# Performance work log

Measured on AMD Instinct MI355X. Metric: run time of the kernel, lower is better.

## Reference

```python
import jax, jax.numpy as jnp
import numpy as np

EPS = 1e-5  # torch BatchNorm1d default eps
O, T, D, H1, H2 = 8, 4, 256, 64, 32


def setup_inputs() -> dict:
    key = jax.random.key(0)
    ks = jax.random.split(key, 8)
    B = 65536
    feature = jax.random.normal(ks[0], (B, D), dtype=jnp.float32)
    treatment = jax.random.randint(ks[1], (B,), 0, T, dtype=jnp.int64)
    s1 = 1.0 / np.sqrt(D)
    s2 = 1.0 / np.sqrt(H1)
    s3 = 1.0 / np.sqrt(H2)
    params = {
        # per (outcome, treatment) expert MLP weights
        'W1': jax.random.uniform(ks[2], (O, T, D, H1), jnp.float32, -s1, s1),
        'b1': jnp.zeros((O, T, H1), jnp.float32),
        'g1': jnp.ones((O, T, H1), jnp.float32),   # BN1 gamma
        'be1': jnp.zeros((O, T, H1), jnp.float32),  # BN1 beta
        'm1': jnp.zeros((O, T, H1), jnp.float32),   # BN1 running mean
        'v1': jnp.ones((O, T, H1), jnp.float32),    # BN1 running var
        'W2': jax.random.uniform(ks[3], (O, T, H1, H2), jnp.float32, -s2, s2),
        'b2': jnp.zeros((O, T, H2), jnp.float32),
        'g2': jnp.ones((O, T, H2), jnp.float32),
        'be2': jnp.zeros((O, T, H2), jnp.float32),
        'm2': jnp.zeros((O, T, H2), jnp.float32),
        'v2': jnp.ones((O, T, H2), jnp.float32),
        'W3': jax.random.uniform(ks[4], (O, T, H2), jnp.float32, -s3, s3),  # final Linear(32,1), squeezed
        'b3': jnp.zeros((O, T), jnp.float32),
    }
    return {'feature': feature, 'treatment': treatment, **params}


def _tlearner_fwd(x, t, W1, b1, g1, be1, m1, v1, W2, b2, g2, be2, m2, v2, W3, b3):
    # Dense evaluation of every (outcome, treatment) expert, then per-row
    # selection by treatment id. Equivalent (in eval mode: BN uses running
    # stats, dropout off) to the masked dispatch of the original module.
    h = jnp.einsum('bd,otdh->both', x, W1) + b1          # [B,O,T,H1]
    h = jax.nn.relu(h)
    h = (h - m1) * jax.lax.rsqrt(v1 + EPS) * g1 + be1    # BN1 (eval)
    h = jnp.einsum('both,othk->botk', h, W2) + b2        # [B,O,T,H2]
    h = jax.nn.relu(h)
    h = (h - m2) * jax.lax.rsqrt(v2 + EPS) * g2 + be2    # BN2 (eval)
    out = jnp.einsum('botk,otk->bot', h, W3) + b3        # [B,O,T]
    idx = t.astype(jnp.int32)[:, None, None]             # [B,1,1]
    return jnp.take_along_axis(out, jnp.broadcast_to(idx, (out.shape[0], O, 1)), axis=2)[..., 0]  # [B,O]


def reference(feature, treatment, W1, b1, g1, be1, m1, v1, W2, b2, g2, be2, m2, v2, W3, b3):
    return _tlearner_fwd(feature, treatment, W1, b1, g1, be1, m1, v1,
                         W2, b2, g2, be2, m2, v2, W3, b3)
```

## Files before the change

kernel.cpp:

```cpp
#include <hip/hip_runtime.h>
#include <cstdint>

typedef short bf16x8 __attribute__((ext_vector_type(8)));
typedef float f32x4 __attribute__((ext_vector_type(4)));

#define NO 8
#define NT 4
#define ND 256
#define NH1 64
#define NH2 32
#define BM 64
#define BNEPS 1e-5f

__device__ __forceinline__ unsigned bfpack2(float a, float b) {
    unsigned ua = __float_as_uint(a), ub = __float_as_uint(b);
    ua = (ua + 0x7FFFu + ((ua >> 16) & 1u)) >> 16;
    ub = (ub + 0x7FFFu + ((ub >> 16) & 1u)) >> 16;
    return ua | (ub << 16);
}


__global__ void k_init(int* __restrict__ ws, int* __restrict__ perm, int n) {
    const int gi = blockIdx.x * blockDim.x + threadIdx.x;
    if (gi < 16) ws[gi] = 0;
    if (gi < n) perm[gi] = -1;
}

__global__ void k_hist(const int* __restrict__ trt, int* __restrict__ cnt, int B) {
    __shared__ int loc[NT];
    const int tid = threadIdx.x;
    if (tid < NT) loc[tid] = 0;
    __syncthreads();
    const int i = blockIdx.x * blockDim.x + tid;
    if (i < B) atomicAdd(&loc[trt[i] & 3], 1);
    __syncthreads();
    if (tid < NT) atomicAdd(&cnt[tid], loc[tid]);
}

__global__ void k_prefix(int* __restrict__ ws) {
    int b = 0;
#pragma unroll
    for (int t = 0; t < NT; ++t) {
        ws[4 + t] = b; ws[12 + t] = b;
        b += (ws[t] + BM - 1) & ~(BM - 1);
    }
    ws[8] = b;
}

__global__ void k_scatter(const int* __restrict__ trt, int* __restrict__ ws,
                          int* __restrict__ perm, int B) {
    __shared__ int loc[NT], gb[NT];
    const int tid = threadIdx.x;
    if (tid < NT) loc[tid] = 0;
    __syncthreads();
    const int i = blockIdx.x * blockDim.x + tid;
    int tt = 0, pos = 0;
    if (i < B) { tt = trt[i] & 3; pos = atomicAdd(&loc[tt], 1); }
    __syncthreads();
    if (tid < NT) gb[tid] = atomicAdd(&ws[12 + tid], loc[tid]);
    __syncthreads();
    if (i < B) perm[gb[tt] + pos] = i;
}

__global__ __launch_bounds__(256) void k_prep(const float* __restrict__ W1,
                                              const float* __restrict__ W2,
                                              unsigned* __restrict__ W1T4,
                                              unsigned* __restrict__ W2T4) {
    const int bid = blockIdx.x, tid = threadIdx.x;
    if (bid < 256) {
        const int gi = bid * 256 + tid;
        const int lane = gi & 63, nt = (gi >> 6) & 31, c = (gi >> 11) & 7, t = gi >> 14;
        const int n16 = lane & 15, kg = lane >> 4;
        const int n = nt * 16 + n16, o = n >> 6, h = n & 63;
        const int k0 = c * 32 + kg * 8;
        const float* src = W1 + ((size_t)(o * NT + t) * ND + k0) * NH1 + h;
        float v[8];
#pragma unroll
        for (int j = 0; j < 8; ++j) v[j] = src[(size_t)j * NH1];
        uint4 q;
        q.x = bfpack2(v[0], v[1]); q.y = bfpack2(v[2], v[3]);
        q.z = bfpack2(v[4], v[5]); q.w = bfpack2(v[6], v[7]);
        ((uint4*)W1T4)[gi] = q;
    } else {
        const int gi = (bid - 256) * 256 + tid;
        const int m16 = gi & 15, kg = (gi >> 4) & 3, ks = (gi >> 6) & 1,
                  kt = (gi >> 7) & 1, o = (gi >> 8) & 7, t = gi >> 11;
        const int k2 = kt * 16 + m16, hb = ks * 32 + kg * 8;
        const float* src = W2 + ((size_t)(o * NT + t) * NH1 + hb) * NH2 + k2;
        float v[8];
#pragma unroll
        for (int j = 0; j < 8; ++j) v[j] = src[(size_t)j * NH2];
        uint4 q;
        q.x = bfpack2(v[0], v[1]); q.y = bfpack2(v[2], v[3]);
        q.z = bfpack2(v[4], v[5]); q.w = bfpack2(v[6], v[7]);
        ((uint4*)W2T4)[gi] = q;
    }
}

__global__ __launch_bounds__(256, 2) void k_main(
    const float* __restrict__ X, const int* __restrict__ ws, const int* __restrict__ perm,
    const unsigned short* __restrict__ W1T, const unsigned short* __restrict__ W2T,
    const float* __restrict__ pb1, const float* __restrict__ pg1, const float* __restrict__ pbe1,
    const float* __restrict__ pm1, const float* __restrict__ pv1,
    const float* __restrict__ pb2, const float* __restrict__ pg2, const float* __restrict__ pbe2,
    const float* __restrict__ pm2, const float* __restrict__ pv2,
    const float* __restrict__ W3, const float* __restrict__ pb3, float* __restrict__ out)
{
    const int m0 = blockIdx.x * BM;
    if (m0 >= ws[8]) return;
    const int t = (m0 >= ws[5]) + (m0 >= ws[6]) + (m0 >= ws[7]);
    const int tid = threadIdx.x;
    const int w = tid >> 6;
    const int l = tid & 63;

    __shared__ __align__(16) char LDS[75776];

    const int rid_reg = perm[m0 + l];
    const int xrow = tid >> 2;
    const int rr = __shfl(rid_reg, xrow);
    const int xdo = (tid & 3) * 8;

    f32x4 acc[8][4];
#pragma unroll
    for (int nt = 0; nt < 8; ++nt)
#pragma unroll
        for (int rt = 0; rt < 4; ++rt) acc[nt][rt] = (f32x4){0.f, 0.f, 0.f, 0.f};

    const char* W1Tt = (const char*)W1T + (size_t)t * 262144;
    const int ln4 = (l >> 4) * 4;

    {
#pragma unroll
        for (int u = 0; u < 8; ++u) {
            const int sl = (u * 4 + w) * 1024 + l * 16;
            __builtin_amdgcn_global_load_lds(
                (const __attribute__((address_space(1))) void*)(W1Tt + sl),
                (__attribute__((address_space(3))) void*)(LDS + sl), 16, 0, 0);
        }
        float4 xa = {0,0,0,0}, xb = {0,0,0,0};
        if (rr >= 0) {
            const float* xp = X + (size_t)rr * ND + xdo;
            xa = *(const float4*)xp; xb = *(const float4*)(xp + 4);
        }
        uint4 q;
        q.x = bfpack2(xa.x, xa.y); q.y = bfpack2(xa.z, xa.w);
        q.z = bfpack2(xb.x, xb.y); q.w = bfpack2(xb.z, xb.w);
        *(uint4*)(LDS + 65536 + xrow * 80 + (tid & 3) * 16) = q;
    }
    __syncthreads();

    int cur = 0;
    for (int c = 0; c < 8; ++c) {
        const int nxt = cur ^ 1;
        float4 xa = {0,0,0,0}, xb = {0,0,0,0};
        if (c < 7) {
            const char* src = W1Tt + (c + 1) * 32768;
#pragma unroll
            for (int u = 0; u < 8; ++u) {
                const int sl = (u * 4 + w) * 1024 + l * 16;
                __builtin_amdgcn_global_load_lds(
                    (const __attribute__((address_space(1))) void*)(src + sl),
                    (__attribute__((address_space(3))) void*)(LDS + nxt * 32768 + sl), 16, 0, 0);
            }
            if (rr >= 0) {
                const float* xp = X + (size_t)rr * ND + (c + 1) * 32 + xdo;
                xa = *(const float4*)xp; xb = *(const float4*)(xp + 4);
            }
        }
        bf16x8 aA[8];
#pragma unroll
        for (int nt = 0; nt < 8; ++nt)
            aA[nt] = *(const bf16x8*)(LDS + cur * 32768 + (w * 8 + nt) * 1024 + l * 16);
#pragma unroll
        for (int rt = 0; rt < 4; ++rt) {
            const bf16x8 bX = *(const bf16x8*)(LDS + 65536 + cur * 5120 +
                                               (rt * 16 + (l & 15)) * 80 + (l >> 4) * 16);
#pragma unroll
            for (int nt = 0; nt < 8; ++nt)
                acc[nt][rt] = __builtin_amdgcn_mfma_f32_16x16x32_bf16(aA[nt], bX, acc[nt][rt], 0, 0, 0);
        }
        if (c < 7) {
            uint4 q;
            q.x = bfpack2(xa.x, xa.y); q.y = bfpack2(xa.z, xa.w);
            q.z = bfpack2(xb.x, xb.y); q.w = bfpack2(xb.z, xb.w);
            *(uint4*)(LDS + 65536 + nxt * 5120 + xrow * 80 + (tid & 3) * 16) = q;
        }
        __syncthreads();
        cur = nxt;
    }

#pragma unroll
    for (int nt = 0; nt < 8; ++nt) {
        const int n0 = (w * 8 + nt) * 16 + ln4;
        const int o = n0 >> 6, h0 = n0 & 63;
        const int pidx = (o * NT + t) * NH1 + h0;
        const float4 b1v = *(const float4*)(pb1 + pidx);
        const float4 g1v = *(const float4*)(pg1 + pidx);
        const float4 be1v = *(const float4*)(pbe1 + pidx);
        const float4 m1v = *(const float4*)(pm1 + pidx);
        const float4 v1v = *(const float4*)(pv1 + pidx);
        float bb[4], sc[4], sh[4];
        bb[0] = b1v.x; sc[0] = g1v.x * rsqrtf(v1v.x + BNEPS); sh[0] = be1v.x - m1v.x * sc[0];
        bb[1] = b1v.y; sc[1] = g1v.y * rsqrtf(v1v.y + BNEPS); sh[1] = be1v.y - m1v.y * sc[1];
        bb[2] = b1v.z; sc[2] = g1v.z * rsqrtf(v1v.z + BNEPS); sh[2] = be1v.z - m1v.z * sc[2];
        bb[3] = b1v.w; sc[3] = g1v.w * rsqrtf(v1v.w + BNEPS); sh[3] = be1v.w - m1v.w * sc[3];
#pragma unroll
        for (int rt = 0; rt < 4; ++rt) {
            const int r = rt * 16 + (l & 15);
            const f32x4 a = acc[nt][rt];
            const float z0 = fmaf(fmaxf(a[0] + bb[0], 0.f), sc[0], sh[0]);
            const float z1 = fmaf(fmaxf(a[1] + bb[1], 0.f), sc[1], sh[1]);
            const float z2 = fmaf(fmaxf(a[2] + bb[2], 0.f), sc[2], sh[2]);
            const float z3 = fmaf(fmaxf(a[3] + bb[3], 0.f), sc[3], sh[3]);
            uint2 pk;
            pk.x = bfpack2(z0, z1); pk.y = bfpack2(z2, z3);
            *(uint2*)(LDS + r * 1024 + (((unsigned)(n0 * 2)) ^ (unsigned)((r & 7) << 4))) = pk;
        }
    }

    bf16x8 aW[2][2][2];
#pragma unroll
    for (int oo = 0; oo < 2; ++oo) {
        const int o = w * 2 + oo;
#pragma unroll
        for (int kt = 0; kt < 2; ++kt)
#pragma unroll
            for (int ks = 0; ks < 2; ++ks)
                aW[oo][kt][ks] = *(const bf16x8*)((const char*)W2T +
                    ((((size_t)t * NO + o) * 2 + kt) * 2 + ks) * 1024 + l * 16);
    }
    f32x4 acc2[2][2][4];
#pragma unroll
    for (int oo = 0; oo < 2; ++oo)
#pragma unroll
        for (int kt = 0; kt < 2; ++kt)
#pragma unroll
            for (int rt2 = 0; rt2 < 4; ++rt2) acc2[oo][kt][rt2] = (f32x4){0.f, 0.f, 0.f, 0.f};

#pragma unroll
    for (int rt2 = 0; rt2 < 4; ++rt2) {
        const int r = rt2 * 16 + (l & 15);
        const unsigned swz = (unsigned)((r & 7) << 4);
#pragma unroll
        for (int ks = 0; ks < 2; ++ks) {
            const int nb = ks * 32 + (l >> 4) * 8;
#pragma unroll
            for (int oo = 0; oo < 2; ++oo) {
                const int n8 = (w * 2 + oo) * 64 + nb;
                const bf16x8 bH = *(const bf16x8*)(LDS + r * 1024 + (((unsigned)(n8 * 2)) ^ swz));
#pragma unroll
                for (int kt = 0; kt < 2; ++kt)
                    acc2[oo][kt][rt2] = __builtin_amdgcn_mfma_f32_16x16x32_bf16(aW[oo][kt][ks], bH, acc2[oo][kt][rt2], 0, 0, 0);
            }
        }
    }

    float p[2][4];
#pragma unroll
    for (int oo = 0; oo < 2; ++oo)
#pragma unroll
        for (int rt2 = 0; rt2 < 4; ++rt2) p[oo][rt2] = 0.f;

#pragma unroll
    for (int oo = 0; oo < 2; ++oo) {
        const int o = w * 2 + oo;
#pragma unroll
        for (int kt = 0; kt < 2; ++kt) {
            const int k2 = kt * 16 + ln4;
            const int pidx = (o * NT + t) * NH2 + k2;
            const float4 b2v = *(const float4*)(pb2 + pidx);
            const float4 g2v = *(const float4*)(pg2 + pidx);
            const float4 be2v = *(const float4*)(pbe2 + pidx);
            const float4 m2v = *(const float4*)(pm2 + pidx);
            const float4 v2v = *(const float4*)(pv2 + pidx);
            const float4 w3v = *(const float4*)(W3 + pidx);
            float bb[4], A3[4], C3[4];
            {
                const float s0 = g2v.x * rsqrtf(v2v.x + BNEPS);
                const float s1 = g2v.y * rsqrtf(v2v.y + BNEPS);
                const float s2 = g2v.z * rsqrtf(v2v.z + BNEPS);
                const float s3 = g2v.w * rsqrtf(v2v.w + BNEPS);
                bb[0] = b2v.x; A3[0] = s0 * w3v.x; C3[0] = (be2v.x - m2v.x * s0) * w3v.x;
                bb[1] = b2v.y; A3[1] = s1 * w3v.y; C3[1] = (be2v.y - m2v.y * s1) * w3v.y;
                bb[2] = b2v.z; A3[2] = s2 * w3v.z; C3[2] = (be2v.z - m2v.z * s2) * w3v.z;
                bb[3] = b2v.w; A3[3] = s3 * w3v.w; C3[3] = (be2v.w - m2v.w * s3) * w3v.w;
            }
#pragma unroll
            for (int rt2 = 0; rt2 < 4; ++rt2) {
                const f32x4 a = acc2[oo][kt][rt2];
                float s = fmaf(fmaxf(a[0] + bb[0], 0.f), A3[0], C3[0]);
                s = fmaf(fmaxf(a[1] + bb[1], 0.f), A3[1], s + C3[1]);
                s = fmaf(fmaxf(a[2] + bb[2], 0.f), A3[2], s + C3[2]);
                s = fmaf(fmaxf(a[3] + bb[3], 0.f), A3[3], s + C3[3]);
                p[oo][rt2] += s;
            }
        }
    }
#pragma unroll
    for (int oo = 0; oo < 2; ++oo)
#pragma unroll
        for (int rt2 = 0; rt2 < 4; ++rt2) {
            float v = p[oo][rt2];
            v += __shfl_xor(v, 16);
            v += __shfl_xor(v, 32);
            p[oo][rt2] = v;
        }

    const int oo_s = l >> 5;
    const int bsel = (l >> 4) & 1;
    const int o_s = w * 2 + oo_s;
    const float b3v = pb3[o_s * NT + t];
    const float v0 = oo_s ? (bsel ? p[1][1] : p[1][0]) : (bsel ? p[0][1] : p[0][0]);
    const float v1 = oo_s ? (bsel ? p[1][3] : p[1][2]) : (bsel ? p[0][3] : p[0][2]);
    const int rg0 = bsel * 16 + (l & 15);
    const int ra = __shfl(rid_reg, rg0);
    const int rb = __shfl(rid_reg, rg0 + 32);
    if (ra >= 0) out[(size_t)ra * NO + o_s] = v0 + b3v;
    if (rb >= 0) out[(size_t)rb * NO + o_s] = v1 + b3v;
}

extern "C" void kernel_launch(void* const* d_in, const int* in_sizes, int n_in,
                              void* d_out, int out_size, void* d_ws, size_t ws_size,
                              hipStream_t stream) {
    const float* X   = (const float*)d_in[0];
    const int* trt   = (const int*)d_in[1];
    const float* W1  = (const float*)d_in[2];
    const float* b1  = (const float*)d_in[3];
    const float* g1  = (const float*)d_in[4];
    const float* be1 = (const float*)d_in[5];
    const float* m1  = (const float*)d_in[6];
    const float* v1  = (const float*)d_in[7];
    const float* W2  = (const float*)d_in[8];
    const float* b2  = (const float*)d_in[9];
    const float* g2  = (const float*)d_in[10];
    const float* be2 = (const float*)d_in[11];
    const float* m2  = (const float*)d_in[12];
    const float* v2  = (const float*)d_in[13];
    const float* W3  = (const float*)d_in[14];
    const float* b3  = (const float*)d_in[15];
    float* out = (float*)d_out;

    const int B = in_sizes[1];
    const int permCap = B + NT * BM;
    int* wsi  = (int*)d_ws;
    int* perm = wsi + 16;
    char* wsb = (char*)d_ws;
    size_t off = 64 + (size_t)permCap * 4;
    off = (off + 15) & ~(size_t)15;
    unsigned* W1T4 = (unsigned*)(wsb + off);
    unsigned* W2T4 = (unsigned*)(wsb + off + 1048576);

    const int nb = (B + 255) / 256;
    const int nbi = (permCap + 255) / 256;
    k_init<<<nbi, 256, 0, stream>>>(wsi, perm, permCap);
    k_hist<<<nb, 256, 0, stream>>>(trt, wsi, B);
    k_prefix<<<1, 1, 0, stream>>>(wsi);
    k_scatter<<<nb, 256, 0, stream>>>(trt, wsi, perm, B);
    k_prep<<<288, 256, 0, stream>>>(W1, W2, W1T4, W2T4);

    const int gx = (B + NT * BM) / BM;
    k_main<<<gx, 256, 0, stream>>>(X, wsi, perm,
                                   (const unsigned short*)W1T4, (const unsigned short*)W2T4,
                                   b1, g1, be1, m1, v1, b2, g2, be2, m2, v2, W3, b3, out);
}
```

Baseline: 68.00 us.

## Stage full X tile in swizzled LDS and read W1 fragments directly from global

Replaces the double-buffered LDS pipeline for W1 and X chunks with a single upfront load of the whole 64x256 bf16 X tile into an XOR-swizzled LDS layout. W1 fragments are now read straight from global memory (L2-cached) inside a fully unrolled K loop, which removes the per-chunk barriers. This is meant to cut synchronization and LDS traffic and shrink the LDS footprint. The cost is that global W1 loads now sit on the MFMA critical path with no explicit prefetch, and the X rows are gathered up front.

```diff
diff --git a/kernel.cpp b/kernel.cpp
--- a/kernel.cpp
+++ b/kernel.cpp
@@ -113,12 +113,26 @@
     const int w = tid >> 6;
     const int l = tid & 63;
 
-    __shared__ __align__(16) char LDS[75776];
+    __shared__ __align__(16) char LDS[65536];
 
     const int rid_reg = perm[m0 + l];
-    const int xrow = tid >> 2;
-    const int rr = __shfl(rid_reg, xrow);
-    const int xdo = (tid & 3) * 8;
+
+    {
+        uint2 xr[16];
+#pragma unroll
+        for (int j = 0; j < 16; ++j) {
+            const int rr = __shfl(rid_reg, w * 16 + j);
+            const int rrow = rr < 0 ? 0 : rr;
+            const float4 xv = *(const float4*)(X + (size_t)rrow * ND + l * 4);
+            xr[j].x = bfpack2(xv.x, xv.y);
+            xr[j].y = bfpack2(xv.z, xv.w);
+        }
+#pragma unroll
+        for (int j = 0; j < 16; ++j) {
+            const int r = w * 16 + j;
+            *(uint2*)(LDS + r * 512 + ((l * 8) ^ ((r & 7) << 4))) = xr[j];
+        }
+    }
 
     f32x4 acc[8][4];
 #pragma unroll
@@ -129,65 +143,25 @@
     const char* W1Tt = (const char*)W1T + (size_t)t * 262144;
     const int ln4 = (l >> 4) * 4;
 
-    {
-#pragma unroll
-        for (int u = 0; u < 8; ++u) {
-            const int sl = (u * 4 + w) * 1024 + l * 16;
-            __builtin_amdgcn_global_load_lds(
-                (const __attribute__((address_space(1))) void*)(W1Tt + sl),
-                (__attribute__((address_space(3))) void*)(LDS + sl), 16, 0, 0);
-        }
-        float4 xa = {0,0,0,0}, xb = {0,0,0,0};
-        if (rr >= 0) {
-            const float* xp = X + (size_t)rr * ND + xdo;
-            xa = *(const float4*)xp; xb = *(const float4*)(xp + 4);
-        }
-        uint4 q;
-        q.x = bfpack2(xa.x, xa.y); q.y = bfpack2(xa.z, xa.w);
-        q.z = bfpack2(xb.x, xb.y); q.w = bfpack2(xb.z, xb.w);
-        *(uint4*)(LDS + 65536 + xrow * 80 + (tid & 3) * 16) = q;
-    }
-    __syncthreads();
-
-    int cur = 0;
+    __syncthreads();
+
+#pragma unroll
     for (int c = 0; c < 8; ++c) {
-        const int nxt = cur ^ 1;
-        float4 xa = {0,0,0,0}, xb = {0,0,0,0};
-        if (c < 7) {
-            const char* src = W1Tt + (c + 1) * 32768;
-#pragma unroll
-            for (int u = 0; u < 8; ++u) {
-                const int sl = (u * 4 + w) * 1024 + l * 16;
-                __builtin_amdgcn_global_load_lds(
-                    (const __attribute__((address_space(1))) void*)(src + sl),
-                    (__attribute__((address_space(3))) void*)(LDS + nxt * 32768 + sl), 16, 0, 0);
-            }
-            if (rr >= 0) {
-                const float* xp = X + (size_t)rr * ND + (c + 1) * 32 + xdo;
-                xa = *(const float4*)xp; xb = *(const float4*)(xp + 4);
-            }
-        }
         bf16x8 aA[8];
 #pragma unroll
         for (int nt = 0; nt < 8; ++nt)
-            aA[nt] = *(const bf16x8*)(LDS + cur * 32768 + (w * 8 + nt) * 1024 + l * 16);
+            aA[nt] = *(const bf16x8*)(W1Tt + c * 32768 + (w * 8 + nt) * 1024 + l * 16);
 #pragma unroll
         for (int rt = 0; rt < 4; ++rt) {
-            const bf16x8 bX = *(const bf16x8*)(LDS + 65536 + cur * 5120 +
-                                               (rt * 16 + (l & 15)) * 80 + (l >> 4) * 16);
+            const int r = rt * 16 + (l & 15);
+            const bf16x8 bX = *(const bf16x8*)(LDS + r * 512 +
+                                               ((c * 64 + (l >> 4) * 16) ^ ((r & 7) << 4)));
 #pragma unroll
             for (int nt = 0; nt < 8; ++nt)
                 acc[nt][rt] = __builtin_amdgcn_mfma_f32_16x16x32_bf16(aA[nt], bX, acc[nt][rt], 0, 0, 0);
         }
-        if (c < 7) {
-            uint4 q;
-            q.x = bfpack2(xa.x, xa.y); q.y = bfpack2(xa.z, xa.w);
-            q.z = bfpack2(xb.x, xb.y); q.w = bfpack2(xb.z, xb.w);
-            *(uint4*)(LDS + 65536 + nxt * 5120 + xrow * 80 + (tid & 3) * 16) = q;
-        }
-        __syncthreads();
-        cur = nxt;
-    }
+    }
+    __syncthreads();
 
 #pragma unroll
     for (int nt = 0; nt < 8; ++nt) {
```

Measured after the change: 70.74 us. 1.04x slower.
